# Kernel tuning notes

Measured on AMD Instinct MI355X. Metric: run time of the kernel, lower is better.

The kernel has to match this reference:

```python
import jax, jax.numpy as jnp
import numpy as np

RADIUS = 0.12   # init_kwargs radius
NSAMPLE = 32    # init_kwargs nsample
USE_XYZ = True  # init_kwargs use_xyz


def ball_query(xyz, new_xyz, radius, nsample):
    """xyz: (B,N,3), new_xyz: (B,M,3) -> idx (B,M,nsample) int32.
    PointNet++ semantics: first `nsample` points (in index order) within
    `radius` of each query; slots past the count are padded with the first
    found index."""
    B, N, _ = xyz.shape
    # squared distances (B, M, N) -- the dominant intermediate
    d2 = jnp.sum((new_xyz[:, :, None, :] - xyz[:, None, :, :]) ** 2, axis=-1)
    mask = d2 < radius * radius
    # score so that earlier in-ball indices have higher score; out-of-ball = 0
    score = jnp.where(mask, (N - jnp.arange(N, dtype=jnp.int32)), 0)
    _, idx = jax.lax.top_k(score, nsample)            # (B, M, nsample)
    valid = jnp.take_along_axis(mask, idx, axis=-1)   # which slots are real hits
    idx = jnp.where(valid, idx, idx[..., :1])         # pad with first found index
    return idx


def group_points(feat, idx):
    """feat: (B,C,N), idx: (B,M,S) -> (B,C,M,S) gather along N."""
    B, C, N = feat.shape
    M, S = idx.shape[1], idx.shape[2]
    idx_flat = jnp.broadcast_to(idx.reshape(B, 1, M * S), (B, C, M * S))
    out = jnp.take_along_axis(feat, idx_flat, axis=2)
    return out.reshape(B, C, M, S)


def setup_inputs() -> dict:
    key = jax.random.key(0)
    k1, k2 = jax.random.split(key)
    B, N, M, C = 4, 8192, 4096, 64
    xyz = jax.random.uniform(k1, (B, N, 3), dtype=jnp.float32)  # points in unit cube
    new_xyz = xyz[:, :M, :]                                      # FPS-like subset of points
    features = jax.random.normal(k2, (B, C, N), dtype=jnp.float32)
    return {"xyz": xyz, "new_xyz": new_xyz, "features": features}


def reference(xyz, new_xyz, features):
    idx = ball_query(xyz, new_xyz, RADIUS, NSAMPLE)             # (B,M,S)
    xyz_t = jnp.transpose(xyz, (0, 2, 1))                        # (B,3,N)
    grouped_xyz = group_points(xyz_t, idx)                       # (B,3,M,S)
    grouped_xyz = grouped_xyz - jnp.transpose(new_xyz, (0, 2, 1))[..., None]
    grouped_feat = group_points(features, idx)                   # (B,C,M,S)
    if USE_XYZ:
        new_features = jnp.concatenate([grouped_xyz, grouped_feat], axis=1)
    else:
        new_features = grouped_feat
    return new_features  # (B, 3+C, M, S)
```

## Files before the change

### kernel.cpp

```cpp
#include <hip/hip_runtime.h>
#include <cstdint>
#include <cstddef>

#define BB 4
#define NN 8192
#define MM 4096
#define CC 64
#define SS 32
#define CH 67
#define NC 512
#define RMARG 0.1201f

__device__ __constant__ float kRR = (float)(0.12 * 0.12);

__device__ __forceinline__ int cell_of(float x, float y, float z) {
    const int ix = min((int)(x * 8.0f), 7);
    const int iy = min((int)(y * 8.0f), 7);
    const int iz = min((int)(z * 8.0f), 7);
    return (ix << 6) + (iy << 3) + iz;
}

__device__ __forceinline__ int block_scan512(int v, int tid, int* wsum) {
    int incl = v;
    #pragma unroll
    for (int d = 1; d < 64; d <<= 1) {
        const int t = __shfl_up(incl, d);
        if ((tid & 63) >= d) incl += t;
    }
    if ((tid & 63) == 63 && tid < NC) wsum[tid >> 6] = incl;
    __syncthreads();
    if (tid < 8) {
        const int ws = wsum[tid];
        int w2 = ws;
        #pragma unroll
        for (int d = 1; d < 8; d <<= 1) {
            const int t = __shfl_up(w2, d);
            if (tid >= d) w2 += t;
        }
        wsum[tid] = w2 - ws;
    }
    __syncthreads();
    return incl + wsum[(tid >> 6) & 7];
}

__global__ __launch_bounds__(1024) void k_prep(
    const float* __restrict__ xyz,
    const float* __restrict__ feat,
    float* __restrict__ ft,
    int* __restrict__ cellStart,
    float4* __restrict__ pk)
{
    __shared__ __align__(16) char smem[64 * 65 * sizeof(float)];
    const int blk = (int)blockIdx.x;
    const int tid = (int)threadIdx.x;

    if (blk < BB) {
        int* sm   = (int*)smem;
        int* cur  = sm + NC;
        int* wsum = cur + NC;
        const int b = blk;

        if (tid < NC) sm[tid] = 0;
        __syncthreads();

        float xs[8], ys[8], zs[8];
        int cl[8];
        const float* __restrict__ xb = xyz + (size_t)b * NN * 3;
        #pragma unroll
        for (int k = 0; k < 8; ++k) {
            const int n = (k << 10) + tid;
            xs[k] = xb[n * 3 + 0];
            ys[k] = xb[n * 3 + 1];
            zs[k] = xb[n * 3 + 2];
            cl[k] = cell_of(xs[k], ys[k], zs[k]);
            atomicAdd(&sm[cl[k]], 1);
        }
        __syncthreads();

        const int v = (tid < NC) ? sm[tid] : 0;
        const int incl = block_scan512(v, tid, wsum);
        if (tid < NC) {
            cellStart[b * (NC + 1) + tid + 1] = incl;
            cur[tid] = incl - v;
            if (tid == 0) cellStart[b * (NC + 1)] = 0;
        }
        __syncthreads();

        #pragma unroll
        for (int k = 0; k < 8; ++k) {
            const int n = (k << 10) + tid;
            const int pos = atomicAdd(&cur[cl[k]], 1);
            pk[b * NN + pos] = make_float4(xs[k], ys[k], zs[k], __int_as_float(n));
        }
    } else {
        float (*tile)[65] = (float(*)[65])smem;
        const int blk2 = blk - BB;
        const int b = blk2 / (NN / 64);
        const int n0 = (blk2 % (NN / 64)) * 64;
        const int tn = tid & 63;
        const int q = tid >> 6;
        const float* __restrict__ fb = feat + (size_t)b * CC * NN;
        #pragma unroll
        for (int k = 0; k < 4; ++k) {
            const int c = (q << 2) + k;
            tile[tn][c] = fb[(size_t)c * NN + n0 + tn];
        }
        __syncthreads();
        float* fo = ft + ((size_t)b * NN + n0) * CC;
        #pragma unroll
        for (int k = 0; k < 4; ++k) {
            const int rn = (q << 2) + k;
            fo[(size_t)rn * CC + tn] = tile[rn][tn];
        }
    }
}

__global__ __launch_bounds__(256) void qg_grid_kernel(
    const float4* __restrict__ pk,
    const int* __restrict__ cellStart,
    const float* __restrict__ ft,
    const float* __restrict__ xyz,
    const float* __restrict__ new_xyz,
    float* __restrict__ out)
{
    __shared__ unsigned int bm[4][2][NN / 32];
    __shared__ int slots_sm[4][2][SS];

    const int tid = (int)threadIdx.x;
    const int lane = tid & 63;
    const int w = tid >> 6;
    const int pair = (int)blockIdx.x * 4 + w;
    const int b = pair >> 11;
    const int m0 = (pair & 2047) << 1;

    #pragma unroll
    for (int k = 0; k < 8; ++k) bm[w][k & 1][((k >> 1) << 6) + lane] = 0u;

    const float* __restrict__ xb = xyz + (size_t)b * NN * 3;
    const float* __restrict__ qb = new_xyz + ((size_t)b * MM + m0) * 3;
    const float cxq[2] = { qb[0], qb[3] };
    const float cyq[2] = { qb[1], qb[4] };
    const float czq[2] = { qb[2], qb[5] };
    const float rr = kRR;

    const int* __restrict__ cs = cellStart + b * (NC + 1);
    const float4* __restrict__ pb = pk + b * NN;

    int Kcq[2];

    #pragma unroll
    for (int q = 0; q < 2; ++q) {
        const float cx = cxq[q], cy = cyq[q], cz = czq[q];
        unsigned int* __restrict__ bitmap = bm[w][q];
        int* __restrict__ slot = slots_sm[w][q];

        const int x0 = max(0, (int)((cx - RMARG) * 8.0f));
        const int x1 = min(7, (int)((cx + RMARG) * 8.0f));
        const int y0 = max(0, (int)((cy - RMARG) * 8.0f));
        const int y1 = min(7, (int)((cy + RMARG) * 8.0f));
        const int z0 = max(0, (int)((cz - RMARG) * 8.0f));
        const int z1 = min(7, (int)((cz + RMARG) * 8.0f));

        const int ny = y1 - y0 + 1;
        const int npair = (x1 - x0 + 1) * ny;
        int begL = 0, endL = 0;
        if (lane < npair) {
            const int px = lane / ny;
            const int py = lane - px * ny;
            const int cb2 = ((x0 + px) << 6) + ((y0 + py) << 3);
            begL = cs[cb2 + z0];
            endL = cs[cb2 + z1 + 1];
        }

        for (int p = 0; p < npair; ++p) {
            const int beg = __shfl(begL, p);
            const int end = __shfl(endL, p);
            for (int off = beg; off < end; off += 64) {
                const int a = off + lane;
                const bool act = a < end;
                const float4 v = pb[act ? a : beg];
                const float dx = __fsub_rn(v.x, cx);
                const float dy = __fsub_rn(v.y, cy);
                const float dz = __fsub_rn(v.z, cz);
                const float d2 = __fadd_rn(__fadd_rn(__fmul_rn(dx, dx), __fmul_rn(dy, dy)),
                                           __fmul_rn(dz, dz));
                if (act && d2 < rr) {
                    const int n = __float_as_int(v.w);
                    atomicOr(&bitmap[n >> 5], 1u << (n & 31));
                }
            }
        }

        const uint4 wv = *reinterpret_cast<const uint4*>(&bitmap[lane << 2]);
        const int pc = __popc(wv.x) + __popc(wv.y) + __popc(wv.z) + __popc(wv.w);
        int incl = pc;
        #pragma unroll
        for (int d = 1; d < 64; d <<= 1) {
            const int t = __shfl_up(incl, d);
            if (lane >= d) incl += t;
        }
        const int K = __shfl(incl, 63);
        int r = incl - pc;
        if (r < SS) {
            const int base = lane << 7;
            unsigned int mw0 = wv.x, mw1 = wv.y, mw2 = wv.z, mw3 = wv.w;
            while (mw0 && r < SS) { slot[r++] = base +  0 + __builtin_ctz(mw0); mw0 &= mw0 - 1; }
            while (mw1 && r < SS) { slot[r++] = base + 32 + __builtin_ctz(mw1); mw1 &= mw1 - 1; }
            while (mw2 && r < SS) { slot[r++] = base + 64 + __builtin_ctz(mw2); mw2 &= mw2 - 1; }
            while (mw3 && r < SS) { slot[r++] = base + 96 + __builtin_ctz(mw3); mw3 &= mw3 - 1; }
        }
        Kcq[q] = (K < SS) ? K : SS;
    }

    const int q = lane >> 5;
    const int s = lane & 31;
    const int Kc = q ? Kcq[1] : Kcq[0];
    int n_of;
    if (Kc == 0) n_of = 0;
    else n_of = slots_sm[w][q][(s < Kc) ? s : 0];

    const size_t plane = (size_t)(MM * SS);
    const size_t obase = ((size_t)b * CH) * plane + (size_t)m0 * SS + lane;

    {
        const float* xr = xb + (size_t)n_of * 3;
        const float gx = __fsub_rn(xr[0], q ? cxq[1] : cxq[0]);
        const float gy = __fsub_rn(xr[1], q ? cyq[1] : cyq[0]);
        const float gz = __fsub_rn(xr[2], q ? czq[1] : czq[0]);
        __builtin_nontemporal_store(gx, &out[obase + 0 * plane]);
        __builtin_nontemporal_store(gy, &out[obase + 1 * plane]);
        __builtin_nontemporal_store(gz, &out[obase + 2 * plane]);
    }
    const float4* fr4 = (const float4*)(ft + ((size_t)b * NN + n_of) * CC);
    #pragma unroll
    for (int half = 0; half < 2; ++half) {
        float4 f[8];
        #pragma unroll
        for (int j = 0; j < 8; ++j) f[j] = fr4[(half << 3) + j];
        #pragma unroll
        for (int j = 0; j < 8; ++j) {
            const int c0 = 3 + (half << 5) + (j << 2);
            __builtin_nontemporal_store(f[j].x, &out[obase + (size_t)(c0 + 0) * plane]);
            __builtin_nontemporal_store(f[j].y, &out[obase + (size_t)(c0 + 1) * plane]);
            __builtin_nontemporal_store(f[j].z, &out[obase + (size_t)(c0 + 2) * plane]);
            __builtin_nontemporal_store(f[j].w, &out[obase + (size_t)(c0 + 3) * plane]);
        }
    }
}

__global__ __launch_bounds__(256) void qg_fused_kernel(
    const float* __restrict__ xyz, const float* __restrict__ new_xyz,
    const float* __restrict__ feat, float* __restrict__ out)
{
    const int wave = (int)((blockIdx.x * blockDim.x + threadIdx.x) >> 6);
    const int lane = (int)(threadIdx.x & 63);
    const int b = wave / MM;
    const int m = wave % MM;

    const float* __restrict__ xb = xyz + (size_t)b * NN * 3;
    const size_t qoff = ((size_t)b * MM + m) * 3;
    const float cx = new_xyz[qoff + 0];
    const float cy = new_xyz[qoff + 1];
    const float cz = new_xyz[qoff + 2];
    const float rr = kRR;

    int my_nb = -1;
    int cnt = 0;

    for (int base = 0; base < NN; base += 512) {
        float px[8], py[8], pz[8];
        #pragma unroll
        for (int k = 0; k < 8; ++k) {
            const int i = base + (k << 6) + lane;
            px[k] = xb[i * 3 + 0]; py[k] = xb[i * 3 + 1]; pz[k] = xb[i * 3 + 2];
        }
        #pragma unroll
        for (int k = 0; k < 8; ++k) {
            const float dx = __fsub_rn(px[k], cx);
            const float dy = __fsub_rn(py[k], cy);
            const float dz = __fsub_rn(pz[k], cz);
            const float d2 = __fadd_rn(__fadd_rn(__fmul_rn(dx, dx), __fmul_rn(dy, dy)),
                                       __fmul_rn(dz, dz));
            const bool hit = d2 < rr;
            const unsigned long long mask = __ballot(hit);
            const int pc = __popcll(mask);
            if (pc) {
                const int rank = cnt + (int)__popcll(mask & ((1ull << lane) - 1ull));
                const int addr = (hit && rank < 63) ? rank : 63;
                const int recv = __builtin_amdgcn_ds_permute(addr << 2,
                                                             base + (k << 6) + lane);
                if (lane >= cnt && lane < SS && (lane - cnt) < pc) my_nb = recv;
                cnt += pc;
                if (cnt >= SS) break;
            }
        }
        if (cnt >= SS) break;
    }

    int first = __shfl(my_nb, 0);
    if (first < 0) first = 0;
    if (lane < SS && my_nb < 0) my_nb = first;
    const int n_of = __shfl(my_nb, lane & 31);

    const int s = lane & 31;
    const int h = lane >> 5;
    const size_t obase = ((size_t)b * CH) * (size_t)(MM * SS) + (size_t)m * SS + s;
    const float* __restrict__ fb = feat + (size_t)b * CC * NN;
    #pragma unroll 2
    for (int cc = 0; cc < CH + 1; cc += 2) {
        const int c = cc + h;
        if (c < CH) {
            float v;
            if (c < 3) {
                const float center = (c == 0) ? cx : (c == 1) ? cy : cz;
                v = __fsub_rn(xb[(size_t)n_of * 3 + c], center);
            } else {
                v = fb[(size_t)(c - 3) * NN + n_of];
            }
            out[obase + (size_t)c * (size_t)(MM * SS)] = v;
        }
    }
}

extern "C" void kernel_launch(void* const* d_in, const int* in_sizes, int n_in,
                              void* d_out, int out_size, void* d_ws, size_t ws_size,
                              hipStream_t stream) {
    const float* xyz     = (const float*)d_in[0];
    const float* new_xyz = (const float*)d_in[1];
    const float* feat    = (const float*)d_in[2];
    float* out = (float*)d_out;

    const size_t ft_b = (size_t)BB * NN * CC * sizeof(float);
    float*  ft     = (float*)d_ws;
    int*    cellSt = (int*)((char*)d_ws + ft_b);
    char*   after  = (char*)(cellSt + BB * (NC + 1));
    float4* pk     = (float4*)(((uintptr_t)after + 15) & ~(uintptr_t)15);
    const size_t need = ((char*)(pk + BB * NN) - (char*)d_ws);

    if (ws_size >= need) {
        k_prep<<<BB + BB * (NN / 64), 1024, 0, stream>>>(xyz, feat, ft, cellSt, pk);
        qg_grid_kernel<<<(BB * MM) / 8, 256, 0, stream>>>(pk, cellSt, ft, xyz,
                                                          new_xyz, out);
    } else {
        qg_fused_kernel<<<(BB * MM) / 4, 256, 0, stream>>>(xyz, new_xyz, feat, out);
    }
}
```

Baseline: 59.21 us.

## Stage grouped outputs through LDS to emit wide 16-byte coalesced stores

Each block now covers eight consecutive queries, so each output channel plane holds 256 contiguous floats per block. The gathered xyz offsets and feature values go into the reused bitmap shared memory first and are then written out as 16-byte vector nontemporal stores instead of scalar 4-byte stores. The per-query counts move to shared memory, and query coordinates are reloaded per thread. In exchange it adds block-wide barriers per channel group, and the feature loop is no longer fully unrolled, which limits overlap of the gather loads.

```diff
diff --git a/kernel.cpp b/kernel.cpp
--- a/kernel.cpp
+++ b/kernel.cpp
@@ -10,6 +10,8 @@
 #define CH 67
 #define NC 512
 #define RMARG 0.1201f
+
+typedef float f32x4 __attribute__((ext_vector_type(4)));
 
 __device__ __constant__ float kRR = (float)(0.12 * 0.12);
 
@@ -123,15 +125,16 @@
     const float* __restrict__ new_xyz,
     float* __restrict__ out)
 {
-    __shared__ unsigned int bm[4][2][NN / 32];
+    __shared__ __align__(16) unsigned int bm[4][2][NN / 32];
     __shared__ int slots_sm[4][2][SS];
+    __shared__ int Kq_sm[8];
 
     const int tid = (int)threadIdx.x;
     const int lane = tid & 63;
     const int w = tid >> 6;
-    const int pair = (int)blockIdx.x * 4 + w;
-    const int b = pair >> 11;
-    const int m0 = (pair & 2047) << 1;
+    const int b = (int)blockIdx.x >> 9;
+    const int m0_blk = ((int)blockIdx.x & 511) << 3;
+    const int m0 = m0_blk + (w << 1);
 
     #pragma unroll
     for (int k = 0; k < 8; ++k) bm[w][k & 1][((k >> 1) << 6) + lane] = 0u;
@@ -145,8 +148,6 @@
 
     const int* __restrict__ cs = cellStart + b * (NC + 1);
     const float4* __restrict__ pb = pk + b * NN;
-
-    int Kcq[2];
 
     #pragma unroll
     for (int q = 0; q < 2; ++q) {
@@ -209,42 +210,57 @@
             while (mw2 && r < SS) { slot[r++] = base + 64 + __builtin_ctz(mw2); mw2 &= mw2 - 1; }
             while (mw3 && r < SS) { slot[r++] = base + 96 + __builtin_ctz(mw3); mw3 &= mw3 - 1; }
         }
-        Kcq[q] = (K < SS) ? K : SS;
-    }
-
-    const int q = lane >> 5;
-    const int s = lane & 31;
-    const int Kc = q ? Kcq[1] : Kcq[0];
-    int n_of;
-    if (Kc == 0) n_of = 0;
-    else n_of = slots_sm[w][q][(s < Kc) ? s : 0];
-
-    const size_t plane = (size_t)(MM * SS);
-    const size_t obase = ((size_t)b * CH) * plane + (size_t)m0 * SS + lane;
+        if (lane == 0) Kq_sm[(w << 1) + q] = (K < SS) ? K : SS;
+    }
+    __syncthreads();
+
+    const int qi = tid >> 5;
+    const int s  = tid & 31;
+    const int w2 = qi >> 1, qq = qi & 1;
+    const int Kc = Kq_sm[qi];
+    const int n_of = (Kc == 0) ? 0 : slots_sm[w2][qq][(s < Kc) ? s : 0];
+    const int m = m0_blk + qi;
+
+    const float* qb2 = new_xyz + ((size_t)b * MM + m) * 3;
+    const float cx2 = qb2[0], cy2 = qb2[1], cz2 = qb2[2];
+
+    float* stage = (float*)bm;
+    const size_t plane = (size_t)MM * SS;
+    const size_t obase0 = ((size_t)b * CH) * plane + (size_t)m0_blk * SS;
 
     {
         const float* xr = xb + (size_t)n_of * 3;
-        const float gx = __fsub_rn(xr[0], q ? cxq[1] : cxq[0]);
-        const float gy = __fsub_rn(xr[1], q ? cyq[1] : cyq[0]);
-        const float gz = __fsub_rn(xr[2], q ? czq[1] : czq[0]);
-        __builtin_nontemporal_store(gx, &out[obase + 0 * plane]);
-        __builtin_nontemporal_store(gy, &out[obase + 1 * plane]);
-        __builtin_nontemporal_store(gz, &out[obase + 2 * plane]);
-    }
+        stage[0 * 256 + tid] = __fsub_rn(xr[0], cx2);
+        stage[1 * 256 + tid] = __fsub_rn(xr[1], cy2);
+        stage[2 * 256 + tid] = __fsub_rn(xr[2], cz2);
+        __syncthreads();
+        #pragma unroll
+        for (int c = 0; c < 3; ++c)
+            __builtin_nontemporal_store(stage[c * 256 + tid],
+                                        &out[obase0 + (size_t)c * plane + tid]);
+        __syncthreads();
+    }
+
     const float4* fr4 = (const float4*)(ft + ((size_t)b * NN + n_of) * CC);
-    #pragma unroll
-    for (int half = 0; half < 2; ++half) {
-        float4 f[8];
-        #pragma unroll
-        for (int j = 0; j < 8; ++j) f[j] = fr4[(half << 3) + j];
-        #pragma unroll
-        for (int j = 0; j < 8; ++j) {
-            const int c0 = 3 + (half << 5) + (j << 2);
-            __builtin_nontemporal_store(f[j].x, &out[obase + (size_t)(c0 + 0) * plane]);
-            __builtin_nontemporal_store(f[j].y, &out[obase + (size_t)(c0 + 1) * plane]);
-            __builtin_nontemporal_store(f[j].z, &out[obase + (size_t)(c0 + 2) * plane]);
-            __builtin_nontemporal_store(f[j].w, &out[obase + (size_t)(c0 + 3) * plane]);
-        }
+    for (int it = 0; it < 8; ++it) {
+        const float4 f0 = fr4[(it << 1) + 0];
+        const float4 f1 = fr4[(it << 1) + 1];
+        stage[0 * 256 + tid] = f0.x; stage[1 * 256 + tid] = f0.y;
+        stage[2 * 256 + tid] = f0.z; stage[3 * 256 + tid] = f0.w;
+        stage[4 * 256 + tid] = f1.x; stage[5 * 256 + tid] = f1.y;
+        stage[6 * 256 + tid] = f1.z; stage[7 * 256 + tid] = f1.w;
+        __syncthreads();
+        #pragma unroll
+        for (int pass = 0; pass < 2; ++pass) {
+            const int idx = (pass << 10) + (tid << 2);
+            const int cc  = idx >> 8;
+            const int pos = idx & 255;
+            const f32x4 v = *(const f32x4*)&stage[cc * 256 + pos];
+            const int c = 3 + (it << 3) + cc;
+            __builtin_nontemporal_store(v,
+                (f32x4*)&out[obase0 + (size_t)c * plane + pos]);
+        }
+        __syncthreads();
     }
 }
 
```

Measured after the change: 61.49 us. +3.8%, slower.
